# Kernel optimization log

Measured on AMD Instinct MI355X. Metric: run time of the kernel, lower is better.

## Reference

```python
import jax, jax.numpy as jnp
import numpy as np

N_NODES = 100000
N_EDGES = 3200000
N_GRAPHS = 64

def setup_inputs() -> dict:
    key = jax.random.key(0)
    ks = jax.random.split(key, 10)
    x = jax.random.normal(ks[0], (N_NODES, 7), dtype=jnp.float32)
    edge_index = jax.random.randint(ks[1], (2, N_EDGES), 0, N_NODES, dtype=jnp.int64)
    batch = jnp.sort(jax.random.randint(ks[2], (N_NODES,), 0, N_GRAPHS, dtype=jnp.int64))
    # Glorot-ish init for weights (values irrelevant for correctness baseline)
    W1 = jax.random.normal(ks[3], (7, 64), dtype=jnp.float32) * 0.3
    b1 = jnp.zeros((64,), dtype=jnp.float32)
    W2 = jax.random.normal(ks[4], (64, 32), dtype=jnp.float32) * 0.12
    b2 = jnp.zeros((32,), dtype=jnp.float32)
    Wl = jax.random.normal(ks[5], (32, 5), dtype=jnp.float32) * 0.17
    bl = jnp.zeros((5,), dtype=jnp.float32)
    return {"x": x, "edge_index": edge_index, "batch": batch,
            "W1": W1, "b1": b1, "W2": W2, "b2": b2, "Wl": Wl, "bl": bl}


def _gcn_conv(x, row, col, W, b, n_nodes):
    """PyG GCNConv: out = D^{-1/2} (A + I) D^{-1/2} X W + b.
    row/col already include self-loops; aggregation at target `col`."""
    h = x @ W                                         # [N, F_out]
    ones = jnp.ones(row.shape[0], dtype=x.dtype)
    deg = jax.ops.segment_sum(ones, col, num_segments=n_nodes)
    dinv = jnp.where(deg > 0, jax.lax.rsqrt(deg), 0.0)
    norm = dinv[row] * dinv[col]                      # [E]
    msg = h[row] * norm[:, None]                      # [E, F_out] gather
    out = jax.ops.segment_sum(msg, col, num_segments=n_nodes)  # scatter-add
    return out + b


def reference(x, edge_index, batch, W1, b1, W2, b2, Wl, bl):
    n = x.shape[0]
    loop = jnp.arange(n, dtype=edge_index.dtype)
    row = jnp.concatenate([edge_index[0], loop])      # add self-loops
    col = jnp.concatenate([edge_index[1], loop])

    h = jax.nn.relu(_gcn_conv(x, row, col, W1, b1, n))
    h = jax.nn.relu(_gcn_conv(h, row, col, W2, b2, n))
    h = h @ Wl + bl                                   # [N, 5]

    # global_mean_pool over graph ids
    sums = jax.ops.segment_sum(h, batch, num_segments=N_GRAPHS)
    cnts = jax.ops.segment_sum(jnp.ones((n,), h.dtype), batch, num_segments=N_GRAPHS)
    return sums / jnp.maximum(cnts, 1.0)[:, None]
```

## Files before the change

kernel.cpp:

```cpp
#include <hip/hip_runtime.h>

#define N_GRAPHS 64
#define EPB 8192
#define MAXBK 1024
#define BSTAGE 16384

#if __has_builtin(__builtin_amdgcn_cvt_pk_f32_fp8) && __has_builtin(__builtin_amdgcn_cvt_pk_fp8_f32)
#define HAS_FP8 1
#else
#define HAS_FP8 0
#endif

typedef float f32x2 __attribute__((ext_vector_type(2)));

__device__ inline float bf2f(unsigned short u) {
    union { unsigned u; float f; } c; c.u = (unsigned)u << 16; return c.f;
}
__device__ inline unsigned short f2bf(float f) {
    union { float f; unsigned u; } c; c.f = f;
    unsigned b = c.u;
    return (unsigned short)((b + 0x7fffu + ((b >> 16) & 1u)) >> 16);
}
__device__ inline void addpair(float& a0, float& a1, unsigned u) {
    union { unsigned x; float f; } lo, hi;
    lo.x = u << 16;
    hi.x = u & 0xffff0000u;
    a0 += lo.f;
    a1 += hi.f;
}

__global__ __launch_bounds__(256) void k_count(
        const int* __restrict__ col, int* __restrict__ cnt,
        int E, int NBLK, int NBK) {
    __shared__ int h[MAXBK];
    for (int t = threadIdx.x; t < NBK; t += 256) h[t] = 0;
    __syncthreads();
    int s = blockIdx.x * EPB, e = min(E, s + EPB);
    int nvec = (e - s) >> 2;
    const uint4* col4 = (const uint4*)(col + s);
    for (int v = threadIdx.x; v < nvec; v += 256) {
        uint4 c = col4[v];
        atomicAdd(&h[c.x >> 8], 1);
        atomicAdd(&h[c.y >> 8], 1);
        atomicAdd(&h[c.z >> 8], 1);
        atomicAdd(&h[c.w >> 8], 1);
    }
    for (int j = s + (nvec << 2) + threadIdx.x; j < e; j += 256)
        atomicAdd(&h[col[j] >> 8], 1);
    __syncthreads();
    for (int b = threadIdx.x; b < NBK; b += 256)
        cnt[(size_t)b * NBLK + blockIdx.x] = h[b];
}

__global__ __launch_bounds__(256) void k_scan_partial(
        const int* __restrict__ in, int* __restrict__ outv,
        int* __restrict__ bsum, int n) {
    __shared__ int lds[256];
    int t = threadIdx.x;
    int base = blockIdx.x * 4096 + t * 16;
    int v[16], s = 0;
#pragma unroll
    for (int q = 0; q < 16; q++) {
        v[q] = (base + q < n) ? in[base + q] : 0;
        s += v[q];
    }
    lds[t] = s;
    __syncthreads();
    for (int d = 1; d < 256; d <<= 1) {
        int tmp = (t >= d) ? lds[t - d] : 0;
        __syncthreads();
        lds[t] += tmp;
        __syncthreads();
    }
    int run = lds[t] - s;
#pragma unroll
    for (int q = 0; q < 16; q++) {
        if (base + q < n) outv[base + q] = run;
        run += v[q];
    }
    if (t == 255) bsum[blockIdx.x] = lds[255];
}

__global__ __launch_bounds__(256) void k_scan_blocks(
        const int* __restrict__ bsum, int* __restrict__ bexcl, int nb) {
    __shared__ int lds[256];
    int t = threadIdx.x;
    int v = (t < nb) ? bsum[t] : 0;
    lds[t] = v;
    __syncthreads();
    for (int d = 1; d < 256; d <<= 1) {
        int tmp = (t >= d) ? lds[t - d] : 0;
        __syncthreads();
        lds[t] += tmp;
        __syncthreads();
    }
    if (t < nb) bexcl[t] = lds[t] - v;
}

__global__ void k_scan_add(int* __restrict__ outv, const int* __restrict__ bexcl,
                           int n, int E) {
    int i = blockIdx.x * blockDim.x + threadIdx.x;
    if (i < n) outv[i] += bexcl[i >> 12];
    if (i == 0) outv[n] = E;
}

__global__ __launch_bounds__(256) void k_binscatter(
        const int* __restrict__ row, const int* __restrict__ col,
        const int* __restrict__ baseA, unsigned int* __restrict__ ebuf,
        int E, int NBLK, int NBK) {
    __shared__ int cur[MAXBK];
    for (int b = threadIdx.x; b < NBK; b += 256)
        cur[b] = baseA[(size_t)b * NBLK + blockIdx.x];
    __syncthreads();
    int s = blockIdx.x * EPB, e = min(E, s + EPB);
    int nvec = (e - s) >> 2;
    const uint4* col4 = (const uint4*)(col + s);
    const uint4* row4 = (const uint4*)(row + s);
    for (int v = threadIdx.x; v < nvec; v += 256) {
        uint4 c = col4[v];
        uint4 r = row4[v];
        int p0 = atomicAdd(&cur[c.x >> 8], 1);
        int p1 = atomicAdd(&cur[c.y >> 8], 1);
        int p2 = atomicAdd(&cur[c.z >> 8], 1);
        int p3 = atomicAdd(&cur[c.w >> 8], 1);
        ebuf[p0] = (r.x << 8) | (c.x & 255u);
        ebuf[p1] = (r.y << 8) | (c.y & 255u);
        ebuf[p2] = (r.z << 8) | (c.z & 255u);
        ebuf[p3] = (r.w << 8) | (c.w & 255u);
    }
    for (int j = s + (nvec << 2) + threadIdx.x; j < e; j += 256) {
        unsigned c = (unsigned)col[j], r = (unsigned)row[j];
        int p = atomicAdd(&cur[c >> 8], 1);
        ebuf[p] = (r << 8) | (c & 255u);
    }
}

__global__ __launch_bounds__(256) void k_bprep(
        const unsigned int* __restrict__ ebuf, const int* __restrict__ baseA,
        const float* __restrict__ x, float* __restrict__ dinv,
        unsigned short* __restrict__ xs, int* __restrict__ off,
        int* __restrict__ srow, int n, int NBLK, int NBK, int E) {
    __shared__ int h[256];
    __shared__ int cur[256];
    __shared__ unsigned stage[BSTAGE];
    int t = threadIdx.x, b = blockIdx.x;
    h[t] = 0;
    __syncthreads();
    int s = baseA[(size_t)b * NBLK];
    int e = baseA[(size_t)(b + 1) * NBLK];
    int m = e - s;
    bool fit = (m <= BSTAGE);
    if (fit) {
        for (int j = t; j < m; j += 256) {
            unsigned rec = ebuf[s + j];
            stage[j] = rec;
            atomicAdd(&h[rec & 255], 1);
        }
    } else {
        for (int j = s + t; j < e; j += 256)
            atomicAdd(&h[ebuf[j] & 255], 1);
    }
    __syncthreads();
    int dg = h[t];
    cur[t] = dg;
    __syncthreads();
    for (int d = 1; d < 256; d <<= 1) {
        int tmp = (t >= d) ? cur[t - d] : 0;
        __syncthreads();
        cur[t] += tmp;
        __syncthreads();
    }
    int myoff = s + cur[t] - dg;
    int node = b * 256 + t;
    if (node < n) {
        off[node] = myoff;
        float d = rsqrtf((float)(dg + 1));
        dinv[node] = d;
        unsigned short r[8];
#pragma unroll
        for (int k = 0; k < 7; k++) r[k] = f2bf(x[(size_t)node * 7 + k] * d);
        r[7] = 0;
        uint4 v;
        v.x = (unsigned)r[0] | ((unsigned)r[1] << 16);
        v.y = (unsigned)r[2] | ((unsigned)r[3] << 16);
        v.z = (unsigned)r[4] | ((unsigned)r[5] << 16);
        v.w = (unsigned)r[6] | ((unsigned)r[7] << 16);
        *(uint4*)(xs + (size_t)node * 8) = v;
    }
    if (b == NBK - 1 && t == 0) off[n] = E;
    __syncthreads();
    cur[t] = myoff;
    __syncthreads();
    if (fit) {
        for (int j = t; j < m; j += 256) {
            unsigned rec = stage[j];
            int p = atomicAdd(&cur[rec & 255], 1);
            srow[p] = (int)(rec >> 8);
        }
    } else {
        for (int j = s + t; j < e; j += 256) {
            unsigned rec = ebuf[j];
            int p = atomicAdd(&cur[rec & 255], 1);
            srow[p] = (int)(rec >> 8);
        }
    }
}

__global__ __launch_bounds__(256) void k_agg1(
        const unsigned short* __restrict__ xs, const float* __restrict__ dinv,
        const int* __restrict__ off, const int* __restrict__ srow,
        float* __restrict__ aggx, int n) {
    int tid = blockIdx.x * blockDim.x + threadIdx.x;
    int c = tid >> 2;
    if (c >= n) return;
    int fp = tid & 3;
    int o0 = off[c], o1 = off[c + 1];
    float a0 = 0.f, a1 = 0.f;
    addpair(a0, a1, *(const unsigned*)(xs + (size_t)c * 8 + fp * 2));
    int j = o0;
    for (; j + 4 <= o1; j += 4) {
        int r0 = srow[j], r1 = srow[j + 1], r2 = srow[j + 2], r3 = srow[j + 3];
        unsigned u0 = *(const unsigned*)(xs + (size_t)r0 * 8 + fp * 2);
        unsigned u1 = *(const unsigned*)(xs + (size_t)r1 * 8 + fp * 2);
        unsigned u2 = *(const unsigned*)(xs + (size_t)r2 * 8 + fp * 2);
        unsigned u3 = *(const unsigned*)(xs + (size_t)r3 * 8 + fp * 2);
        addpair(a0, a1, u0); addpair(a0, a1, u1);
        addpair(a0, a1, u2); addpair(a0, a1, u3);
    }
    for (; j < o1; j++)
        addpair(a0, a1, *(const unsigned*)(xs + (size_t)srow[j] * 8 + fp * 2));
    float d = dinv[c];
    aggx[(size_t)c * 8 + fp * 2]     = a0 * d;
    aggx[(size_t)c * 8 + fp * 2 + 1] = a1 * d;
}

__global__ __launch_bounds__(256) void k_mlp1(
        const float* __restrict__ aggx, const float* __restrict__ dinv,
        const float* __restrict__ W1, const float* __restrict__ b1,
        const float* __restrict__ W2,
        unsigned int* __restrict__ hs, int n) {
    __shared__ float sW1[7 * 64];
    __shared__ float sb1[64];
    __shared__ float sW2[64 * 32];
    for (int t = threadIdx.x; t < 7 * 64; t += blockDim.x) sW1[t] = W1[t];
    for (int t = threadIdx.x; t < 64; t += blockDim.x) sb1[t] = b1[t];
    for (int t = threadIdx.x; t < 64 * 32; t += blockDim.x) sW2[t] = W2[t];
    __syncthreads();

    int i = blockIdx.x * blockDim.x + threadIdx.x;
    if (i >= n) return;

    float a[7];
#pragma unroll
    for (int k = 0; k < 7; k++) a[k] = aggx[(size_t)i * 8 + k];

    float acc[32];
#pragma unroll
    for (int m = 0; m < 32; m++) acc[m] = 0.f;

    for (int j = 0; j < 64; j++) {
        float v = sb1[j];
#pragma unroll
        for (int k = 0; k < 7; k++) v += a[k] * sW1[k * 64 + j];
        v = fmaxf(v, 0.f);
#pragma unroll
        for (int m = 0; m < 32; m++) acc[m] += v * sW2[j * 32 + m];
    }
    float d = dinv[i];
#if HAS_FP8
    float sc = d * 8.f;
    unsigned w[8];
#pragma unroll
    for (int q = 0; q < 8; q++) {
        unsigned t0 = (unsigned)__builtin_amdgcn_cvt_pk_fp8_f32(
            acc[4 * q] * sc, acc[4 * q + 1] * sc, 0, false);
        w[q] = (unsigned)__builtin_amdgcn_cvt_pk_fp8_f32(
            acc[4 * q + 2] * sc, acc[4 * q + 3] * sc, (int)t0, true);
    }
    uint4* o = (uint4*)(hs + (size_t)i * 8);
    o[0] = make_uint4(w[0], w[1], w[2], w[3]);
    o[1] = make_uint4(w[4], w[5], w[6], w[7]);
#else
    unsigned up[16];
#pragma unroll
    for (int m = 0; m < 16; m++)
        up[m] = (unsigned)f2bf(acc[2 * m] * d) |
                ((unsigned)f2bf(acc[2 * m + 1] * d) << 16);
    uint4* o = (uint4*)(hs + (size_t)i * 16);
    o[0] = make_uint4(up[0],  up[1],  up[2],  up[3]);
    o[1] = make_uint4(up[4],  up[5],  up[6],  up[7]);
    o[2] = make_uint4(up[8],  up[9],  up[10], up[11]);
    o[3] = make_uint4(up[12], up[13], up[14], up[15]);
#endif
}

__global__ __launch_bounds__(256) void k_agg2(
        const unsigned int* __restrict__ hs, const float* __restrict__ dinv,
        const int* __restrict__ off, const int* __restrict__ srow,
        float* __restrict__ agg2, int n) {
    int tid = blockIdx.x * blockDim.x + threadIdx.x;
    int c = tid >> 2;
    if (c >= n) return;
    int fp = tid & 3;
    int o0 = off[c], o1 = off[c + 1];
    float a0 = 0.f, a1 = 0.f, a2 = 0.f, a3 = 0.f;
    float a4 = 0.f, a5 = 0.f, a6 = 0.f, a7 = 0.f;
#if HAS_FP8
    auto dec = [&](uint2 u) {
        f32x2 p0 = __builtin_amdgcn_cvt_pk_f32_fp8((int)u.x, false);
        f32x2 p1 = __builtin_amdgcn_cvt_pk_f32_fp8((int)u.x, true);
        f32x2 p2 = __builtin_amdgcn_cvt_pk_f32_fp8((int)u.y, false);
        f32x2 p3 = __builtin_amdgcn_cvt_pk_f32_fp8((int)u.y, true);
        a0 += p0.x; a1 += p0.y; a2 += p1.x; a3 += p1.y;
        a4 += p2.x; a5 += p2.y; a6 += p3.x; a7 += p3.y;
    };
    dec(*(const uint2*)(hs + (size_t)c * 8 + fp * 2));
    int j = o0;
    for (; j + 4 <= o1; j += 4) {
        int r0 = srow[j], r1 = srow[j + 1], r2 = srow[j + 2], r3 = srow[j + 3];
        uint2 u0 = *(const uint2*)(hs + (size_t)r0 * 8 + fp * 2);
        uint2 u1 = *(const uint2*)(hs + (size_t)r1 * 8 + fp * 2);
        uint2 u2 = *(const uint2*)(hs + (size_t)r2 * 8 + fp * 2);
        uint2 u3 = *(const uint2*)(hs + (size_t)r3 * 8 + fp * 2);
        dec(u0); dec(u1); dec(u2); dec(u3);
    }
    for (; j < o1; j++)
        dec(*(const uint2*)(hs + (size_t)srow[j] * 8 + fp * 2));
    float d = dinv[c] * 0.125f;
#else
    auto dec = [&](uint4 u) {
        addpair(a0, a1, u.x); addpair(a2, a3, u.y);
        addpair(a4, a5, u.z); addpair(a6, a7, u.w);
    };
    dec(*(const uint4*)(hs + (size_t)c * 16 + fp * 4));
    int j = o0;
    for (; j + 4 <= o1; j += 4) {
        int r0 = srow[j], r1 = srow[j + 1], r2 = srow[j + 2], r3 = srow[j + 3];
        uint4 u0 = *(const uint4*)(hs + (size_t)r0 * 16 + fp * 4);
        uint4 u1 = *(const uint4*)(hs + (size_t)r1 * 16 + fp * 4);
        uint4 u2 = *(const uint4*)(hs + (size_t)r2 * 16 + fp * 4);
        uint4 u3 = *(const uint4*)(hs + (size_t)r3 * 16 + fp * 4);
        dec(u0); dec(u1); dec(u2); dec(u3);
    }
    for (; j < o1; j++)
        dec(*(const uint4*)(hs + (size_t)srow[j] * 16 + fp * 4));
    float d = dinv[c];
#endif
    float4* o = (float4*)(agg2 + (size_t)c * 32 + fp * 8);
    o[0] = make_float4(a0 * d, a1 * d, a2 * d, a3 * d);
    o[1] = make_float4(a4 * d, a5 * d, a6 * d, a7 * d);
}

__global__ void k_gstart(const int* __restrict__ batch, int* __restrict__ gstart,
                         int n) {
    int i = blockIdx.x * blockDim.x + threadIdx.x;
    if (i >= n) return;
    int g = batch[i];
    int gp = (i == 0) ? -1 : batch[i - 1];
    for (int q = gp + 1; q <= g; q++) gstart[q] = i;
    if (i == n - 1)
        for (int q = g + 1; q <= N_GRAPHS; q++) gstart[q] = n;
}

__global__ __launch_bounds__(256) void k_pool(
        const float* __restrict__ agg2, const float* __restrict__ b2,
        const int* __restrict__ gstart, float* __restrict__ psum) {
    int g = blockIdx.x >> 3, ch = blockIdx.x & 7;
    int s = gstart[g], e = gstart[g + 1];
    int cnt = e - s;
    int per = (cnt + 7) >> 3;
    int cs = s + ch * per, ce = min(e, cs + per);

    int t = threadIdx.x;
    int fq = t & 7, nl = t >> 3;
    const float4* b2q4 = (const float4*)b2;
    float4 bq = b2q4[fq];
    float4 acc = make_float4(0.f, 0.f, 0.f, 0.f);
    for (int i = cs + nl; i < ce; i += 32) {
        float4 v = *(const float4*)(agg2 + (size_t)i * 32 + fq * 4);
        acc.x += fmaxf(v.x + bq.x, 0.f);
        acc.y += fmaxf(v.y + bq.y, 0.f);
        acc.z += fmaxf(v.z + bq.z, 0.f);
        acc.w += fmaxf(v.w + bq.w, 0.f);
    }
#pragma unroll
    for (int m = 8; m < 64; m <<= 1) {
        acc.x += __shfl_xor(acc.x, m);
        acc.y += __shfl_xor(acc.y, m);
        acc.z += __shfl_xor(acc.z, m);
        acc.w += __shfl_xor(acc.w, m);
    }
    __shared__ float4 part[4][8];
    int w = t >> 6, lane = t & 63;
    if (lane < 8) part[w][lane] = acc;
    __syncthreads();
    if (t < 8) {
        float4 p0 = part[0][t], p1 = part[1][t], p2 = part[2][t], p3 = part[3][t];
        float4 r;
        r.x = p0.x + p1.x + p2.x + p3.x;
        r.y = p0.y + p1.y + p2.y + p3.y;
        r.z = p0.z + p1.z + p2.z + p3.z;
        r.w = p0.w + p1.w + p2.w + p3.w;
        *(float4*)(psum + ((size_t)((g << 3) + ch)) * 32 + t * 4) = r;
    }
}

__global__ void k_out(const float* __restrict__ psum, const int* __restrict__ gstart,
                      const float* __restrict__ Wl, const float* __restrict__ bl,
                      float* __restrict__ out) {
    int t = blockIdx.x * blockDim.x + threadIdx.x;
    if (t >= N_GRAPHS * 5) return;
    int g = t / 5, o = t % 5;
    float c = (float)max(gstart[g + 1] - gstart[g], 1);
    float acc = 0.f;
#pragma unroll
    for (int m = 0; m < 32; m++) {
        float s = 0.f;
#pragma unroll
        for (int ch = 0; ch < 8; ch++)
            s += psum[((size_t)((g << 3) + ch)) * 32 + m];
        acc += s * Wl[m * 5 + o];
    }
    out[t] = acc / c + bl[o];
}

extern "C" void kernel_launch(void* const* d_in, const int* in_sizes, int n_in,
                              void* d_out, int out_size, void* d_ws, size_t ws_size,
                              hipStream_t stream) {
    const float* x     = (const float*)d_in[0];
    const int*   ei    = (const int*)d_in[1];
    const int*   batch = (const int*)d_in[2];
    const float* W1    = (const float*)d_in[3];
    const float* b1    = (const float*)d_in[4];
    const float* W2    = (const float*)d_in[5];
    const float* b2    = (const float*)d_in[6];
    const float* Wl    = (const float*)d_in[7];
    const float* bl    = (const float*)d_in[8];
    float* out = (float*)d_out;

    const int n = in_sizes[0] / 7;
    const int E = in_sizes[1] / 2;
    const int* row = ei;
    const int* col = ei + E;

    const int NBK  = (n + 255) >> 8;
    const int NBLK = (E + EPB - 1) / EPB;
    const int NT   = NBK * NBLK;

    char* p = (char*)d_ws;
    auto alloc = [&](size_t bytes) -> char* {
        char* r = p;
        p += (bytes + 255) & ~(size_t)255;
        return r;
    };
    int*   cnt    = (int*)  alloc((size_t)NT * 4);
    int*   baseA  = (int*)  alloc((size_t)(NT + 1) * 4);
    unsigned int* ebuf = (unsigned int*)alloc((size_t)E * 4);
    int*   srow   = (int*)  alloc((size_t)E * 4);
    float* dinv   = (float*)alloc((size_t)n * 4);
    int*   off    = (int*)  alloc((size_t)(n + 1) * 4);
    unsigned short* xs = (unsigned short*)alloc((size_t)n * 8 * 2);
    float* aggx   = (float*)alloc((size_t)n * 8 * 4);
    unsigned int* hs = (unsigned int*)alloc((size_t)n * 16 * 4);
    float* agg2   = (float*)alloc((size_t)n * 32 * 4);
    int*   bsum2  = (int*)  alloc(256 * 4);
    int*   bexcl2 = (int*)  alloc(256 * 4);
    int*   gstart = (int*)  alloc((N_GRAPHS + 1) * 4);
    float* psum   = (float*)alloc((size_t)N_GRAPHS * 8 * 32 * 4);

    const int BT = 256;
    int nb_n     = (n + BT - 1) / BT;
    int nb_scanT = (NT + 4095) / 4096;
    int nb_quad  = (n * 4 + BT - 1) / BT;

    k_count       <<<NBLK, BT, 0, stream>>>(col, cnt, E, NBLK, NBK);
    k_scan_partial<<<nb_scanT, BT, 0, stream>>>(cnt, baseA, bsum2, NT);
    k_scan_blocks <<<1, BT, 0, stream>>>(bsum2, bexcl2, nb_scanT);
    k_scan_add    <<<(NT + BT) / BT, BT, 0, stream>>>(baseA, bexcl2, NT, E);
    k_binscatter  <<<NBLK, BT, 0, stream>>>(row, col, baseA, ebuf, E, NBLK, NBK);
    k_bprep       <<<NBK, BT, 0, stream>>>(ebuf, baseA, x, dinv, xs, off, srow,
                                           n, NBLK, NBK, E);
    k_gstart      <<<nb_n, BT, 0, stream>>>(batch, gstart, n);

    k_agg1        <<<nb_quad, BT, 0, stream>>>(xs, dinv, off, srow, aggx, n);
    k_mlp1        <<<nb_n, BT, 0, stream>>>(aggx, dinv, W1, b1, W2, hs, n);
    k_agg2        <<<nb_quad, BT, 0, stream>>>(hs, dinv, off, srow, agg2, n);
    k_pool        <<<N_GRAPHS * 8, BT, 0, stream>>>(agg2, b2, gstart, psum);
    k_out         <<<1, 320, 0, stream>>>(psum, gstart, Wl, bl, out);
}
```

Measured before the change: 156.7 us.

## Fuse count and bin-scatter into one pass with block-local bucket layout

```diff
diff --git a/kernel.cpp b/kernel.cpp
--- a/kernel.cpp
+++ b/kernel.cpp
@@ -2,7 +2,6 @@
 
 #define N_GRAPHS 64
 #define EPB 8192
-#define MAXBK 1024
 #define BSTAGE 16384
 
 #if __has_builtin(__builtin_amdgcn_cvt_pk_f32_fp8) && __has_builtin(__builtin_amdgcn_cvt_pk_fp8_f32)
@@ -29,136 +28,150 @@
     a1 += hi.f;
 }
 
-__global__ __launch_bounds__(256) void k_count(
-        const int* __restrict__ col, int* __restrict__ cnt,
+__global__ __launch_bounds__(256) void k_count2(
+        const int* __restrict__ row, const int* __restrict__ col,
+        int* __restrict__ meta, unsigned int* __restrict__ ebuf,
         int E, int NBLK, int NBK) {
-    __shared__ int h[MAXBK];
-    for (int t = threadIdx.x; t < NBK; t += 256) h[t] = 0;
+    __shared__ int h[512];
+    __shared__ int scn[512];
+    int t = threadIdx.x;
+    int i0 = t, i1 = t + 256;
+    h[i0] = 0; h[i1] = 0;
     __syncthreads();
     int s = blockIdx.x * EPB, e = min(E, s + EPB);
     int nvec = (e - s) >> 2;
     const uint4* col4 = (const uint4*)(col + s);
-    for (int v = threadIdx.x; v < nvec; v += 256) {
+    const uint4* row4 = (const uint4*)(row + s);
+    for (int v = t; v < nvec; v += 256) {
         uint4 c = col4[v];
         atomicAdd(&h[c.x >> 8], 1);
         atomicAdd(&h[c.y >> 8], 1);
         atomicAdd(&h[c.z >> 8], 1);
         atomicAdd(&h[c.w >> 8], 1);
     }
-    for (int j = s + (nvec << 2) + threadIdx.x; j < e; j += 256)
+    for (int j = s + (nvec << 2) + t; j < e; j += 256)
         atomicAdd(&h[col[j] >> 8], 1);
     __syncthreads();
-    for (int b = threadIdx.x; b < NBK; b += 256)
-        cnt[(size_t)b * NBLK + blockIdx.x] = h[b];
-}
-
-__global__ __launch_bounds__(256) void k_scan_partial(
-        const int* __restrict__ in, int* __restrict__ outv,
-        int* __restrict__ bsum, int n) {
-    __shared__ int lds[256];
-    int t = threadIdx.x;
-    int base = blockIdx.x * 4096 + t * 16;
-    int v[16], s = 0;
-#pragma unroll
-    for (int q = 0; q < 16; q++) {
-        v[q] = (base + q < n) ? in[base + q] : 0;
-        s += v[q];
-    }
-    lds[t] = s;
-    __syncthreads();
-    for (int d = 1; d < 256; d <<= 1) {
-        int tmp = (t >= d) ? lds[t - d] : 0;
-        __syncthreads();
-        lds[t] += tmp;
-        __syncthreads();
-    }
-    int run = lds[t] - s;
-#pragma unroll
-    for (int q = 0; q < 16; q++) {
-        if (base + q < n) outv[base + q] = run;
-        run += v[q];
-    }
-    if (t == 255) bsum[blockIdx.x] = lds[255];
-}
-
-__global__ __launch_bounds__(256) void k_scan_blocks(
-        const int* __restrict__ bsum, int* __restrict__ bexcl, int nb) {
-    __shared__ int lds[256];
-    int t = threadIdx.x;
-    int v = (t < nb) ? bsum[t] : 0;
-    lds[t] = v;
-    __syncthreads();
-    for (int d = 1; d < 256; d <<= 1) {
-        int tmp = (t >= d) ? lds[t - d] : 0;
-        __syncthreads();
-        lds[t] += tmp;
-        __syncthreads();
-    }
-    if (t < nb) bexcl[t] = lds[t] - v;
-}
-
-__global__ void k_scan_add(int* __restrict__ outv, const int* __restrict__ bexcl,
-                           int n, int E) {
-    int i = blockIdx.x * blockDim.x + threadIdx.x;
-    if (i < n) outv[i] += bexcl[i >> 12];
-    if (i == 0) outv[n] = E;
-}
-
-__global__ __launch_bounds__(256) void k_binscatter(
-        const int* __restrict__ row, const int* __restrict__ col,
-        const int* __restrict__ baseA, unsigned int* __restrict__ ebuf,
-        int E, int NBLK, int NBK) {
-    __shared__ int cur[MAXBK];
-    for (int b = threadIdx.x; b < NBK; b += 256)
-        cur[b] = baseA[(size_t)b * NBLK + blockIdx.x];
-    __syncthreads();
-    int s = blockIdx.x * EPB, e = min(E, s + EPB);
-    int nvec = (e - s) >> 2;
-    const uint4* col4 = (const uint4*)(col + s);
-    const uint4* row4 = (const uint4*)(row + s);
-    for (int v = threadIdx.x; v < nvec; v += 256) {
+    scn[i0] = h[i0]; scn[i1] = h[i1];
+    __syncthreads();
+    for (int d = 1; d < 512; d <<= 1) {
+        int v0 = (i0 >= d) ? scn[i0 - d] : 0;
+        int v1 = (i1 >= d) ? scn[i1 - d] : 0;
+        __syncthreads();
+        scn[i0] += v0; scn[i1] += v1;
+        __syncthreads();
+    }
+    int* mrow = meta + (size_t)blockIdx.x * NBK;
+    if (i0 < NBK) { int c0 = h[i0], l0 = scn[i0] - c0; mrow[i0] = (l0 << 16) | c0; }
+    if (i1 < NBK) { int c1 = h[i1], l1 = scn[i1] - c1; mrow[i1] = (l1 << 16) | c1; }
+    __syncthreads();
+    h[i0] = s + scn[i0] - h[i0];
+    h[i1] = s + scn[i1] - h[i1];
+    __syncthreads();
+    for (int v = t; v < nvec; v += 256) {
         uint4 c = col4[v];
         uint4 r = row4[v];
-        int p0 = atomicAdd(&cur[c.x >> 8], 1);
-        int p1 = atomicAdd(&cur[c.y >> 8], 1);
-        int p2 = atomicAdd(&cur[c.z >> 8], 1);
-        int p3 = atomicAdd(&cur[c.w >> 8], 1);
+        int p0 = atomicAdd(&h[c.x >> 8], 1);
+        int p1 = atomicAdd(&h[c.y >> 8], 1);
+        int p2 = atomicAdd(&h[c.z >> 8], 1);
+        int p3 = atomicAdd(&h[c.w >> 8], 1);
         ebuf[p0] = (r.x << 8) | (c.x & 255u);
         ebuf[p1] = (r.y << 8) | (c.y & 255u);
         ebuf[p2] = (r.z << 8) | (c.z & 255u);
         ebuf[p3] = (r.w << 8) | (c.w & 255u);
     }
-    for (int j = s + (nvec << 2) + threadIdx.x; j < e; j += 256) {
+    for (int j = s + (nvec << 2) + t; j < e; j += 256) {
         unsigned c = (unsigned)col[j], r = (unsigned)row[j];
-        int p = atomicAdd(&cur[c >> 8], 1);
+        int p = atomicAdd(&h[c >> 8], 1);
         ebuf[p] = (r << 8) | (c & 255u);
     }
 }
 
+__global__ __launch_bounds__(256) void k_bsum(
+        const int* __restrict__ meta, int* __restrict__ btot,
+        int NBLK, int NBK) {
+    __shared__ int lds[256];
+    int b = blockIdx.x, t = threadIdx.x;
+    int sum = 0;
+    for (int k = t; k < NBLK; k += 256)
+        sum += meta[(size_t)k * NBK + b] & 0xffff;
+    lds[t] = sum;
+    __syncthreads();
+    for (int d = 128; d > 0; d >>= 1) {
+        if (t < d) lds[t] += lds[t + d];
+        __syncthreads();
+    }
+    if (t == 0) btot[b] = lds[0];
+}
+
+__global__ __launch_bounds__(512) void k_bscan(
+        const int* __restrict__ btot, int* __restrict__ bbase, int NBK) {
+    __shared__ int lds[512];
+    int t = threadIdx.x;
+    int v = (t < NBK) ? btot[t] : 0;
+    lds[t] = v;
+    __syncthreads();
+    for (int d = 1; d < 512; d <<= 1) {
+        int tmp = (t >= d) ? lds[t - d] : 0;
+        __syncthreads();
+        lds[t] += tmp;
+        __syncthreads();
+    }
+    if (t < NBK) bbase[t] = lds[t] - v;
+}
+
 __global__ __launch_bounds__(256) void k_bprep(
-        const unsigned int* __restrict__ ebuf, const int* __restrict__ baseA,
-        const float* __restrict__ x, float* __restrict__ dinv,
-        unsigned short* __restrict__ xs, int* __restrict__ off,
-        int* __restrict__ srow, int n, int NBLK, int NBK, int E) {
+        const unsigned int* __restrict__ ebuf, const int* __restrict__ meta,
+        const int* __restrict__ bbase, const float* __restrict__ x,
+        float* __restrict__ dinv, unsigned short* __restrict__ xs,
+        int* __restrict__ off, int* __restrict__ srow,
+        int n, int NBLK, int NBK, int E) {
     __shared__ int h[256];
     __shared__ int cur[256];
+    __shared__ int cnts[512];
+    __shared__ int locs[512];
+    __shared__ int scn[512];
     __shared__ unsigned stage[BSTAGE];
     int t = threadIdx.x, b = blockIdx.x;
+    int i0 = t, i1 = t + 256;
     h[t] = 0;
-    __syncthreads();
-    int s = baseA[(size_t)b * NBLK];
-    int e = baseA[(size_t)(b + 1) * NBLK];
-    int m = e - s;
-    bool fit = (m <= BSTAGE);
+    cnts[i0] = 0; cnts[i1] = 0;
+    __syncthreads();
+    for (int k = t; k < NBLK; k += 256) {
+        int m = meta[(size_t)k * NBK + b];
+        cnts[k] = m & 0xffff;
+        locs[k] = m >> 16;
+    }
+    __syncthreads();
+    scn[i0] = cnts[i0]; scn[i1] = cnts[i1];
+    __syncthreads();
+    for (int d = 1; d < 512; d <<= 1) {
+        int v0 = (i0 >= d) ? scn[i0 - d] : 0;
+        int v1 = (i1 >= d) ? scn[i1 - d] : 0;
+        __syncthreads();
+        scn[i0] += v0; scn[i1] += v1;
+        __syncthreads();
+    }
+    int mtot = scn[511];
+    bool fit = (mtot <= BSTAGE);
     if (fit) {
-        for (int j = t; j < m; j += 256) {
-            unsigned rec = ebuf[s + j];
-            stage[j] = rec;
-            atomicAdd(&h[rec & 255], 1);
+        for (int k = t; k < NBLK; k += 256) {
+            int cnt = cnts[k];
+            const unsigned* src = ebuf + (size_t)k * EPB + locs[k];
+            int dst = scn[k] - cnt;
+            for (int q = 0; q < cnt; q++) {
+                unsigned rec = src[q];
+                stage[dst + q] = rec;
+                atomicAdd(&h[rec & 255], 1);
+            }
         }
     } else {
-        for (int j = s + t; j < e; j += 256)
-            atomicAdd(&h[ebuf[j] & 255], 1);
+        for (int k = t; k < NBLK; k += 256) {
+            int cnt = cnts[k];
+            const unsigned* src = ebuf + (size_t)k * EPB + locs[k];
+            for (int q = 0; q < cnt; q++)
+                atomicAdd(&h[src[q] & 255], 1);
+        }
     }
     __syncthreads();
     int dg = h[t];
@@ -170,7 +183,8 @@
         cur[t] += tmp;
         __syncthreads();
     }
-    int myoff = s + cur[t] - dg;
+    int base = bbase[b];
+    int myoff = base + cur[t] - dg;
     int node = b * 256 + t;
     if (node < n) {
         off[node] = myoff;
@@ -192,16 +206,20 @@
     cur[t] = myoff;
     __syncthreads();
     if (fit) {
-        for (int j = t; j < m; j += 256) {
+        for (int j = t; j < mtot; j += 256) {
             unsigned rec = stage[j];
             int p = atomicAdd(&cur[rec & 255], 1);
             srow[p] = (int)(rec >> 8);
         }
     } else {
-        for (int j = s + t; j < e; j += 256) {
-            unsigned rec = ebuf[j];
-            int p = atomicAdd(&cur[rec & 255], 1);
-            srow[p] = (int)(rec >> 8);
+        for (int k = t; k < NBLK; k += 256) {
+            int cnt = cnts[k];
+            const unsigned* src = ebuf + (size_t)k * EPB + locs[k];
+            for (int q = 0; q < cnt; q++) {
+                unsigned rec = src[q];
+                int p = atomicAdd(&cur[rec & 255], 1);
+                srow[p] = (int)(rec >> 8);
+            }
         }
     }
 }
@@ -445,7 +463,6 @@
 
     const int NBK  = (n + 255) >> 8;
     const int NBLK = (E + EPB - 1) / EPB;
-    const int NT   = NBK * NBLK;
 
     char* p = (char*)d_ws;
     auto alloc = [&](size_t bytes) -> char* {
@@ -453,38 +470,34 @@
         p += (bytes + 255) & ~(size_t)255;
         return r;
     };
-    int*   cnt    = (int*)  alloc((size_t)NT * 4);
-    int*   baseA  = (int*)  alloc((size_t)(NT + 1) * 4);
+    int*   meta   = (int*)  alloc((size_t)NBLK * NBK * 4);
     unsigned int* ebuf = (unsigned int*)alloc((size_t)E * 4);
     int*   srow   = (int*)  alloc((size_t)E * 4);
+    int*   btot   = (int*)  alloc(512 * 4);
+    int*   bbase  = (int*)  alloc(512 * 4);
     float* dinv   = (float*)alloc((size_t)n * 4);
     int*   off    = (int*)  alloc((size_t)(n + 1) * 4);
     unsigned short* xs = (unsigned short*)alloc((size_t)n * 8 * 2);
     float* aggx   = (float*)alloc((size_t)n * 8 * 4);
     unsigned int* hs = (unsigned int*)alloc((size_t)n * 16 * 4);
     float* agg2   = (float*)alloc((size_t)n * 32 * 4);
-    int*   bsum2  = (int*)  alloc(256 * 4);
-    int*   bexcl2 = (int*)  alloc(256 * 4);
     int*   gstart = (int*)  alloc((N_GRAPHS + 1) * 4);
     float* psum   = (float*)alloc((size_t)N_GRAPHS * 8 * 32 * 4);
 
     const int BT = 256;
-    int nb_n     = (n + BT - 1) / BT;
-    int nb_scanT = (NT + 4095) / 4096;
-    int nb_quad  = (n * 4 + BT - 1) / BT;
-
-    k_count       <<<NBLK, BT, 0, stream>>>(col, cnt, E, NBLK, NBK);
-    k_scan_partial<<<nb_scanT, BT, 0, stream>>>(cnt, baseA, bsum2, NT);
-    k_scan_blocks <<<1, BT, 0, stream>>>(bsum2, bexcl2, nb_scanT);
-    k_scan_add    <<<(NT + BT) / BT, BT, 0, stream>>>(baseA, bexcl2, NT, E);
-    k_binscatter  <<<NBLK, BT, 0, stream>>>(row, col, baseA, ebuf, E, NBLK, NBK);
-    k_bprep       <<<NBK, BT, 0, stream>>>(ebuf, baseA, x, dinv, xs, off, srow,
-                                           n, NBLK, NBK, E);
-    k_gstart      <<<nb_n, BT, 0, stream>>>(batch, gstart, n);
-
-    k_agg1        <<<nb_quad, BT, 0, stream>>>(xs, dinv, off, srow, aggx, n);
-    k_mlp1        <<<nb_n, BT, 0, stream>>>(aggx, dinv, W1, b1, W2, hs, n);
-    k_agg2        <<<nb_quad, BT, 0, stream>>>(hs, dinv, off, srow, agg2, n);
-    k_pool        <<<N_GRAPHS * 8, BT, 0, stream>>>(agg2, b2, gstart, psum);
-    k_out         <<<1, 320, 0, stream>>>(psum, gstart, Wl, bl, out);
-}
+    int nb_n    = (n + BT - 1) / BT;
+    int nb_quad = (n * 4 + BT - 1) / BT;
+
+    k_count2 <<<NBLK, BT, 0, stream>>>(row, col, meta, ebuf, E, NBLK, NBK);
+    k_bsum   <<<NBK, BT, 0, stream>>>(meta, btot, NBLK, NBK);
+    k_bscan  <<<1, 512, 0, stream>>>(btot, bbase, NBK);
+    k_bprep  <<<NBK, BT, 0, stream>>>(ebuf, meta, bbase, x, dinv, xs, off, srow,
+                                      n, NBLK, NBK, E);
+    k_gstart <<<nb_n, BT, 0, stream>>>(batch, gstart, n);
+
+    k_agg1   <<<nb_quad, BT, 0, stream>>>(xs, dinv, off, srow, aggx, n);
+    k_mlp1   <<<nb_n, BT, 0, stream>>>(aggx, dinv, W1, b1, W2, hs, n);
+    k_agg2   <<<nb_quad, BT, 0, stream>>>(hs, dinv, off, srow, agg2, n);
+    k_pool   <<<N_GRAPHS * 8, BT, 0, stream>>>(agg2, b2, gstart, psum);
+    k_out    <<<1, 320, 0, stream>>>(psum, gstart, Wl, bl, out);
+}
```

After: 149.3 us. 1.05x faster.
